# Kernel tuning notes

Hardware: AMD Instinct MI355X
Metric: run time of the kernel (lower is better)

Reference implementation:

```python
import jax, jax.numpy as jnp
import numpy as np

B, C, N = 8, 256, 2048
NMOD = 5  # time, space, time_cor, space_cor, global_res


def _attn(x, y, Wqk, Vw, Vb, Tw, Tb):
    """Offset self-attention (PCT-style). x, y: [B, C, N].
    q/k share the same 1x1-conv weight Wqk; v and trans convs have bias.
    softmax over last axis, then L1 renorm over axis=1 of the [B,N,N] map.
    """
    x_q = jnp.einsum('oc,bcn->bno', Wqk, y)           # [B,N,C]
    x_k = jnp.einsum('oc,bcn->bon', Wqk, x)           # [B,C,N]
    x_v = jnp.einsum('oc,bcn->bon', Vw, x) + Vb[:, None]
    att = jax.nn.softmax(jnp.einsum('bnc,bcm->bnm', x_q, x_k), axis=-1)
    att = att / (1e-07 + att.sum(axis=1, keepdims=True))
    x_r = jnp.einsum('bcn,bnm->bcm', x_v, att)        # [B,C,N]
    x_r = jax.nn.relu(jnp.einsum('oc,bcn->bon', Tw, x - x_r) + Tb[:, None])
    return x + x_r


def setup_inputs() -> dict:
    key = jax.random.key(0)
    ks = jax.random.split(key, 6)
    s = 1.0 / np.sqrt(C)
    return {
        'x':   jax.random.normal(ks[0], (B, 3, C, N), dtype=jnp.float32),
        'Wqk': jax.random.normal(ks[1], (NMOD, C, C), dtype=jnp.float32) * s,
        'Vw':  jax.random.normal(ks[2], (NMOD, C, C), dtype=jnp.float32) * s,
        'Vb':  jax.random.normal(ks[3], (NMOD, C), dtype=jnp.float32) * s,
        'Tw':  jax.random.normal(ks[4], (NMOD, C, C), dtype=jnp.float32) * s,
        'Tb':  jax.random.normal(ks[5], (NMOD, C), dtype=jnp.float32) * s,
    }


def reference(x, Wqk, Vw, Vb, Tw, Tb):
    time_x, mid, space_x = x[:, 0], x[:, 1], x[:, 2]

    def A(i, xx, yy):
        return _attn(xx, yy, Wqk[i], Vw[i], Vb[i], Tw[i], Tb[i])

    time_att = A(0, time_x, time_x)
    space_att = A(1, space_x, space_x)
    time_cor = A(2, time_x, space_x)
    space_cor = A(3, space_x, time_x)
    global_feat = A(4, mid, mid)

    time_update = jnp.tanh(time_att * jax.nn.sigmoid(time_cor))
    space_update = jnp.tanh(space_att * jax.nn.sigmoid(space_cor))
    g_sig = jax.nn.sigmoid(global_feat)
    global_residual = jax.nn.sigmoid(time_update * g_sig + space_update * g_sig)
    return mid + global_residual * jnp.tanh(global_feat)
```

## Files before the change

### kernel.cpp

```cpp
#include <hip/hip_runtime.h>
#include <math.h>

#define BB 8
#define CC 256
#define NN 2048

static const size_t NC  = (size_t)NN * CC;
static const size_t CN  = (size_t)CC * NN;

typedef unsigned short u16;
typedef __attribute__((ext_vector_type(8))) short short8;
typedef __attribute__((ext_vector_type(4))) float f32x4;

__device__ __forceinline__ float bf2f(u16 v) {
    union { unsigned int u; float f; } t; t.u = ((unsigned int)v) << 16; return t.f;
}
__device__ __forceinline__ u16 f2bf(float f) {
    union { float f; unsigned int u; } t; t.f = f;
    return (u16)((t.u + 0x7fffu + ((t.u >> 16) & 1u)) >> 16);
}
__device__ __forceinline__ float sigf(float x) { return 1.0f / (1.0f + expf(-x)); }

__device__ __forceinline__ size_t til(int r, int c, int tpr) {
    return (((size_t)((r >> 4) * tpr + (c >> 5))) << 9)
         + (size_t)((r & 15) << 5) + (size_t)(c & 31);
}

__device__ __forceinline__ void stage_tile(const u16* gtile, u16* ldst, int lane) {
    const u16* src = gtile + (lane & 15) * 32 + (lane >> 4) * 8;
    __builtin_amdgcn_global_load_lds(
        (const __attribute__((address_space(1))) void*)src,
        (__attribute__((address_space(3))) void*)ldst, 16, 0, 0);
}
#define WAITV(n) asm volatile("s_waitcnt vmcnt(" #n ")" ::: "memory")

__global__ __launch_bounds__(256) void cast_w(const float* __restrict__ in,
                                              u16* __restrict__ outp)
{
    const int mat = blockIdx.y;
    const int idx = blockIdx.x * 256 + threadIdx.x;
    const int c = idx >> 6, k = (idx & 63) << 2;
    const float4 v = *(const float4*)&in[(size_t)mat * (CC * CC) + (size_t)c * CC + k];
    ushort4 p;
    p.x = f2bf(v.x); p.y = f2bf(v.y); p.z = f2bf(v.z); p.w = f2bf(v.w);
    *(ushort4*)&outp[(size_t)mat * (CC * CC) + til(c, k, CC / 32)] = p;
}

__global__ __launch_bounds__(256) void tcast_x(const float* __restrict__ in,
                                               u16* __restrict__ out)
{
    const int z = blockIdx.z;
    const float* I = in + (size_t)z * CN;
    u16* O = out + (size_t)z * NC;
    const int c0 = blockIdx.y * 64, n0 = blockIdx.x * 64;
    const int tx = threadIdx.x & 15, ty = threadIdx.x >> 4;

    __shared__ float t[64][68];

    #pragma unroll
    for (int cc = 0; cc < 64; cc += 16) {
        const int c = ty + cc;
        *(float4*)&t[c][tx * 4] = *(const float4*)&I[(size_t)(c0 + c) * NN + n0 + tx * 4];
    }
    __syncthreads();
    #pragma unroll
    for (int nn2 = 0; nn2 < 64; nn2 += 16) {
        const int n = n0 + ty + nn2;
        const int c = c0 + tx * 4;
        ushort4 p;
        p.x = f2bf(t[tx * 4 + 0][ty + nn2]);
        p.y = f2bf(t[tx * 4 + 1][ty + nn2]);
        p.z = f2bf(t[tx * 4 + 2][ty + nn2]);
        p.w = f2bf(t[tx * 4 + 3][ty + nn2]);
        *(ushort4*)&O[til(n, c, 8)] = p;
    }
}

struct QkvP {
    const u16* w[12]; const u16* x[12]; u16* out[12];
    const float* bias[12]; int isv[12];
};

__global__ __launch_bounds__(256) void conv_qkv(QkvP P)
{
    const int z = blockIdx.z, job = z >> 3, b = z & 7;
    const int isv = P.isv[job];
    const u16* Wp = P.w[job];
    const u16* Xp = P.x[job] + (size_t)b * (3 * NC);
    const int n0 = blockIdx.x * 128, c0 = blockIdx.y * 128;
    const int lane = threadIdx.x & 63, wave = threadIdx.x >> 6;
    const int l15 = lane & 15, lg = lane >> 4;
    const int rA = (wave >> 1) * 64, rB = (wave & 1) * 64;

    const u16* Ab = isv ? Xp : Wp;
    const u16* Bb = isv ? Wp : Xp;
    const int Ar0 = (isv ? n0 : c0) + rA;
    const int Br0 = (isv ? c0 : n0) + rB;

    const u16* ap[4]; const u16* bp[4];
    #pragma unroll
    for (int i = 0; i < 4; i++) {
        ap[i] = Ab + til(Ar0 + i * 16 + l15, lg * 8, 8);
        bp[i] = Bb + til(Br0 + i * 16 + l15, lg * 8, 8);
    }

    f32x4 acc[4][4] = {};
    #pragma unroll 2
    for (int kc = 0; kc < 8; kc++) {
        short8 av[4], bv[4];
        #pragma unroll
        for (int i = 0; i < 4; i++) av[i] = *(const short8*)(ap[i] + kc * 512);
        #pragma unroll
        for (int i = 0; i < 4; i++) bv[i] = *(const short8*)(bp[i] + kc * 512);
        #pragma unroll
        for (int i = 0; i < 4; i++)
            #pragma unroll
            for (int j = 0; j < 4; j++)
                acc[i][j] = __builtin_amdgcn_mfma_f32_16x16x32_bf16(av[i], bv[j], acc[i][j], 0, 0, 0);
    }

    if (!isv) {
        u16* Ot = P.out[job] + (size_t)b * NC;
        #pragma unroll
        for (int i = 0; i < 4; i++) {
            const int c = c0 + rA + i * 16 + lg * 4;
            #pragma unroll
            for (int j = 0; j < 4; j++) {
                const int n = n0 + rB + j * 16 + l15;
                ushort4 p;
                p.x = f2bf(acc[i][j][0]); p.y = f2bf(acc[i][j][1]);
                p.z = f2bf(acc[i][j][2]); p.w = f2bf(acc[i][j][3]);
                *(ushort4*)&Ot[til(n, c, 8)] = p;
            }
        }
    } else {
        u16* Ov = P.out[job] + (size_t)b * CN;
        const float* bias = P.bias[job];
        #pragma unroll
        for (int j = 0; j < 4; j++) {
            const int c = c0 + rB + j * 16 + l15;
            const float bi = bias[c];
            #pragma unroll
            for (int i = 0; i < 4; i++) {
                const int n = n0 + rA + i * 16 + lg * 4;
                ushort4 p;
                p.x = f2bf(acc[i][j][0] + bi); p.y = f2bf(acc[i][j][1] + bi);
                p.z = f2bf(acc[i][j][2] + bi); p.w = f2bf(acc[i][j][3] + bi);
                *(ushort4*)&Ov[til(c, n, 64)] = p;
            }
        }
    }
}

__global__ __launch_bounds__(256) void conv_t2(
    const u16* __restrict__ W, const u16* __restrict__ Dt,
    const float* __restrict__ bias, const u16* __restrict__ Xts,
    u16* __restrict__ O)
{
    const int bid = blockIdx.x;
    const int b = bid & 7;
    const int rest = bid >> 3;
    const int cy = rest & 1, nx = rest >> 1;
    const int n0 = nx * 128, c0 = cy * 128;
    const int lane = threadIdx.x & 63, wave = threadIdx.x >> 6;
    const int l15 = lane & 15, lg = lane >> 4;
    const int wc = (wave >> 1) * 64, wn = (wave & 1) * 64;

    const u16* Xp = Dt + (size_t)b * NC;
    const u16* ap[4]; const u16* bp[4];
    #pragma unroll
    for (int i = 0; i < 4; i++) {
        ap[i] = W  + til(c0 + wc + i * 16 + l15, lg * 8, 8);
        bp[i] = Xp + til(n0 + wn + i * 16 + l15, lg * 8, 8);
    }

    f32x4 acc[4][4] = {};
    #pragma unroll 2
    for (int kc = 0; kc < 8; kc++) {
        short8 av[4], bv[4];
        #pragma unroll
        for (int i = 0; i < 4; i++) av[i] = *(const short8*)(ap[i] + kc * 512);
        #pragma unroll
        for (int i = 0; i < 4; i++) bv[i] = *(const short8*)(bp[i] + kc * 512);
        #pragma unroll
        for (int i = 0; i < 4; i++)
            #pragma unroll
            for (int j = 0; j < 4; j++)
                acc[i][j] = __builtin_amdgcn_mfma_f32_16x16x32_bf16(av[i], bv[j], acc[i][j], 0, 0, 0);
    }

    const u16* Xtb = Xts + (size_t)b * (3 * NC);
    u16* Ob = O + (size_t)b * CN;
    #pragma unroll
    for (int i = 0; i < 4; i++) {
        const int cb = c0 + wc + i * 16 + lg * 4;
        #pragma unroll
        for (int j = 0; j < 4; j++) {
            const int n = n0 + wn + j * 16 + l15;
            const ushort4 xv = *(const ushort4*)&Xtb[til(n, cb, 8)];
            const u16 xa[4] = { xv.x, xv.y, xv.z, xv.w };
            #pragma unroll
            for (int r = 0; r < 4; r++) {
                const int c = cb + r;
                const float v = bf2f(xa[r]) + fmaxf(acc[i][j][r] + bias[c], 0.0f);
                Ob[til(c, n, 64)] = f2bf(v);
            }
        }
    }
}

__global__ __launch_bounds__(1024) void attn_mfma6(
    const u16* __restrict__ Q, const u16* __restrict__ K,
    u16* __restrict__ Sout, float* __restrict__ CPb)
{
    const int bid = blockIdx.x;
    const int b = bid & 7;
    const int nblk = bid >> 3;
    const int n0 = nblk * 32;
    const int tid = threadIdx.x, lane = tid & 63, wave = tid >> 6;
    const int l15 = lane & 15, lg = lane >> 4;

    const u16* Qt = Q + (size_t)b * NC;
    const u16* Kt = K + (size_t)b * NC;

    __shared__ u16 KL[16 * 8 * 512];
    __shared__ u16 QL[16 * 512];
    __shared__ float red[16][32];
    __shared__ float rowstat[32];

    stage_tile(Qt + ((size_t)((n0 >> 4) + (wave >> 3)) * 8 + (wave & 7)) * 512,
               &QL[wave * 512], lane);
    u16* kw = &KL[wave * 4096];
    #pragma unroll
    for (int p = 0; p < 6; p++)
        stage_tile(Kt + ((size_t)(wave * 8 + (p & 7)) * 8 + (p >> 3)) * 512,
                   &kw[p * 512], lane);
    __syncthreads();

    f32x4 acc[2][8];
    #pragma unroll
    for (int g = 0; g < 2; g++)
        #pragma unroll
        for (int t = 0; t < 8; t++) acc[g][t] = (f32x4){0.f, 0.f, 0.f, 0.f};

    const int roff = lg * 128 + l15 * 8;

    #pragma unroll
    for (int kc = 0; kc < 8; kc++) {
        const short8 a0 = *(const short8*)&QL[kc * 512 + roff];
        const short8 a1 = *(const short8*)&QL[(8 + kc) * 512 + roff];
        #pragma unroll
        for (int t = 0; t < 8; t++) {
            const int i = kc * 8 + t;
            if (i < 58) { WAITV(5); } else if (i == 58) { WAITV(0); }
            const short8 bf = *(const short8*)&kw[(i & 7) * 512 + roff];
            if (i + 6 < 64) {
                const int j = i + 6;
                stage_tile(Kt + ((size_t)(wave * 8 + (j & 7)) * 8 + (j >> 3)) * 512,
                           &kw[(j & 7) * 512], lane);
            }
            __builtin_amdgcn_s_setprio(1);
            acc[0][t] = __builtin_amdgcn_mfma_f32_16x16x32_bf16(a0, bf, acc[0][t], 0, 0, 0);
            acc[1][t] = __builtin_amdgcn_mfma_f32_16x16x32_bf16(a1, bf, acc[1][t], 0, 0, 0);
            __builtin_amdgcn_s_setprio(0);
        }
    }

    float pm[2][4];
    #pragma unroll
    for (int g = 0; g < 2; g++)
        #pragma unroll
        for (int r = 0; r < 4; r++) {
            float m = acc[g][0][r];
            #pragma unroll
            for (int t = 1; t < 8; t++) m = fmaxf(m, acc[g][t][r]);
            #pragma unroll
            for (int o = 1; o <= 8; o <<= 1) m = fmaxf(m, __shfl_xor(m, o));
            pm[g][r] = m;
        }
    if (l15 == 0) {
        #pragma unroll
        for (int g = 0; g < 2; g++)
            #pragma unroll
            for (int r = 0; r < 4; r++) red[wave][g * 16 + lg * 4 + r] = pm[g][r];
    }
    __syncthreads();
    if (tid < 32) {
        float m = red[0][tid];
        #pragma unroll
        for (int w = 1; w < 16; w++) m = fmaxf(m, red[w][tid]);
        rowstat[tid] = m;
    }
    __syncthreads();

    float rm[2][4], ps[2][4];
    #pragma unroll
    for (int g = 0; g < 2; g++)
        #pragma unroll
        for (int r = 0; r < 4; r++) { rm[g][r] = rowstat[g * 16 + lg * 4 + r]; ps[g][r] = 0.f; }
    __syncthreads();

    #pragma unroll
    for (int g = 0; g < 2; g++)
        #pragma unroll
        for (int t = 0; t < 8; t++)
            #pragma unroll
            for (int r = 0; r < 4; r++) {
                const float e = __expf(acc[g][t][r] - rm[g][r]);
                acc[g][t][r] = e; ps[g][r] += e;
            }
    #pragma unroll
    for (int g = 0; g < 2; g++)
        #pragma unroll
        for (int r = 0; r < 4; r++)
            #pragma unroll
            for (int o = 1; o <= 8; o <<= 1) ps[g][r] += __shfl_xor(ps[g][r], o);
    if (l15 == 0) {
        #pragma unroll
        for (int g = 0; g < 2; g++)
            #pragma unroll
            for (int r = 0; r < 4; r++) red[wave][g * 16 + lg * 4 + r] = ps[g][r];
    }
    __syncthreads();
    if (tid < 32) {
        float s = red[0][tid];
        #pragma unroll
        for (int w = 1; w < 16; w++) s += red[w][tid];
        rowstat[tid] = 1.0f / s;
    }
    __syncthreads();

    float rv[2][4];
    #pragma unroll
    for (int g = 0; g < 2; g++)
        #pragma unroll
        for (int r = 0; r < 4; r++) rv[g][r] = rowstat[g * 16 + lg * 4 + r];

    u16* sb = Sout + (size_t)b * NN * NN;
    u16* sbg[2];
    #pragma unroll
    for (int g = 0; g < 2; g++)
        sbg[g] = sb + (size_t)((n0 >> 3) + g * 2 + (lg >> 1)) * (NN * 8) + (lg & 1) * 4;
    float* cpb = CPb + ((size_t)b * 64 + nblk) * NN;

    #pragma unroll
    for (int t = 0; t < 8; t++) {
        const int m = wave * 128 + t * 16 + l15;
        float cs = 0.0f;
        #pragma unroll
        for (int g = 0; g < 2; g++) {
            const float v0 = acc[g][t][0] * rv[g][0], v1 = acc[g][t][1] * rv[g][1];
            const float v2 = acc[g][t][2] * rv[g][2], v3 = acc[g][t][3] * rv[g][3];
            ushort4 pk;
            pk.x = f2bf(v0); pk.y = f2bf(v1); pk.z = f2bf(v2); pk.w = f2bf(v3);
            *(ushort4*)&sbg[g][(size_t)m * 8] = pk;
            cs += v0 + v1 + v2 + v3;
        }
        cs += __shfl_xor(cs, 16);
        cs += __shfl_xor(cs, 32);
        if (lane < 16) cpb[m] = cs;
    }
}

__global__ __launch_bounds__(256) void csum_kernel(const float* __restrict__ cp,
                                                   float* __restrict__ cs)
{
    const int b  = blockIdx.y;
    const int ml = threadIdx.x & 63;
    const int m  = blockIdx.x * 64 + ml;
    const int g0 = threadIdx.x >> 6;
    float s = 0.0f;
    for (int g = g0; g < 64; g += 4)
        s += cp[((size_t)b * 64 + g) * NN + m];
    __shared__ float red[4][64];
    red[g0][ml] = s;
    __syncthreads();
    if (threadIdx.x < 64) {
        cs[(size_t)b * NN + blockIdx.x * 64 + threadIdx.x] =
            red[0][threadIdx.x] + red[1][threadIdx.x] +
            red[2][threadIdx.x] + red[3][threadIdx.x];
    }
}

__global__ __launch_bounds__(256) void pv_mfma(
    const u16* __restrict__ V, const u16* __restrict__ S,
    const float* __restrict__ CSb, const u16* __restrict__ Xts,
    u16* __restrict__ DTo)
{
    const int bid = blockIdx.x;
    const int b = bid & 7;
    const int r2 = bid >> 3;
    const int cy = r2 & 1, mx = r2 >> 1;
    const int m0b = mx * 64, c0 = cy * 128;
    const int lane = threadIdx.x & 63, wave = threadIdx.x >> 6;
    const int wc = (wave >> 1) * 64, wm = (wave & 1) * 32;
    const int l15 = lane & 15, lg = lane >> 4;

    const u16* Vm = V + (size_t)b * CN;
    const u16* Sm = S + (size_t)b * NN * NN;

    f32x4 acc[4][2] = {};
    const u16* vp[4]; const u16* sp[2];
    #pragma unroll
    for (int ai = 0; ai < 4; ai++)
        vp[ai] = Vm + til(c0 + wc + ai * 16 + l15, lg * 8, 64);
    #pragma unroll
    for (int bj = 0; bj < 2; bj++)
        sp[bj] = Sm + ((size_t)lg * NN + m0b + wm + bj * 16 + l15) * 8;

    #pragma unroll 2
    for (int kc = 0; kc < 64; kc++) {
        short8 a[4], s2[2];
        #pragma unroll
        for (int ai = 0; ai < 4; ai++) { a[ai] = *(const short8*)vp[ai]; vp[ai] += 512; }
        #pragma unroll
        for (int bj = 0; bj < 2; bj++) { s2[bj] = *(const short8*)sp[bj]; sp[bj] += (size_t)4 * NN * 8; }
        #pragma unroll
        for (int ai = 0; ai < 4; ai++)
            #pragma unroll
            for (int bj = 0; bj < 2; bj++)
                acc[ai][bj] = __builtin_amdgcn_mfma_f32_16x16x32_bf16(a[ai], s2[bj], acc[ai][bj], 0, 0, 0);
    }

    const u16* Xtb = Xts + (size_t)b * (3 * NC);
    u16* Dtb = DTo + (size_t)b * NC;

    #pragma unroll
    for (int bj = 0; bj < 2; bj++) {
        const int m = m0b + wm + bj * 16 + l15;
        const float inv = 1.0f / (1e-7f + CSb[(size_t)b * NN + m]);
        #pragma unroll
        for (int ai = 0; ai < 4; ai++) {
            const int c = c0 + wc + ai * 16 + lg * 4;
            const size_t ad = til(m, c, 8);
            const ushort4 xv = *(const ushort4*)&Xtb[ad];
            ushort4 pk;
            pk.x = f2bf(bf2f(xv.x) - acc[ai][bj][0] * inv);
            pk.y = f2bf(bf2f(xv.y) - acc[ai][bj][1] * inv);
            pk.z = f2bf(bf2f(xv.z) - acc[ai][bj][2] * inv);
            pk.w = f2bf(bf2f(xv.w) - acc[ai][bj][3] * inv);
            *(ushort4*)&Dtb[ad] = pk;
        }
    }
}

__global__ __launch_bounds__(256) void ew_update_t(u16* __restrict__ A,
                                                   const u16* __restrict__ Bv)
{
    const size_t e = ((size_t)blockIdx.x * 256 + threadIdx.x) * 8;
    short8 a = *(const short8*)&A[e];
    const short8 b = *(const short8*)&Bv[e];
    #pragma unroll
    for (int j = 0; j < 8; j++) {
        const float f = tanhf(bf2f((u16)a[j]) * sigf(bf2f((u16)b[j])));
        a[j] = (short)f2bf(f);
    }
    *(short8*)&A[e] = a;
}

__global__ __launch_bounds__(256) void ew_final_t(
    const u16* __restrict__ TU, const u16* __restrict__ SU,
    const u16* __restrict__ G, const float* __restrict__ x,
    float* __restrict__ OUT)
{
    const size_t e = ((size_t)blockIdx.x * 256 + threadIdx.x) * 8;
    const int b = (int)(e / CN);
    const size_t r = e - (size_t)b * CN;
    const int tile = (int)(r >> 9), win = (int)(r & 511);
    const int row = win >> 5, col = win & 31;
    const int c = (tile >> 6) * 16 + row;
    const int n = (tile & 63) * 32 + col;

    const size_t lin = ((size_t)b * 3 + 1) * CN + (size_t)c * NN + n;
    const float4 m0 = *(const float4*)&x[lin];
    const float4 m1 = *(const float4*)&x[lin + 4];
    const float mid[8] = { m0.x, m0.y, m0.z, m0.w, m1.x, m1.y, m1.z, m1.w };

    const short8 tu = *(const short8*)&TU[e];
    const short8 su = *(const short8*)&SU[e];
    const short8 g  = *(const short8*)&G[e];

    float o[8];
    #pragma unroll
    for (int j = 0; j < 8; j++) {
        const float gg = bf2f((u16)g[j]);
        o[j] = mid[j] + sigf((bf2f((u16)tu[j]) + bf2f((u16)su[j])) * sigf(gg)) * tanhf(gg);
    }
    float* op = OUT + (size_t)b * CN + (size_t)c * NN + n;
    *(float4*)op       = (float4){o[0], o[1], o[2], o[3]};
    *(float4*)(op + 4) = (float4){o[4], o[5], o[6], o[7]};
}

extern "C" void kernel_launch(void* const* d_in, const int* in_sizes, int n_in,
                              void* d_out, int out_size, void* d_ws, size_t ws_size,
                              hipStream_t stream)
{
    const float* x   = (const float*)d_in[0];
    const float* Wqk = (const float*)d_in[1];
    const float* Vw  = (const float*)d_in[2];
    const float* VbF = (const float*)d_in[3];
    const float* Tw  = (const float*)d_in[4];
    const float* TbF = (const float*)d_in[5];
    float* out = (float*)d_out;

    const int mxs[5] = {0, 2, 0, 2, 1};
    const int mys[5] = {0, 2, 2, 0, 1};
    const int qjob[5] = {0, 1, 5, 6, 4};
    const int q_wi[7] = {0, 1, 2, 3, 4, 2, 3};
    const int q_xi[7] = {0, 2, 0, 2, 1, 2, 0};

    const size_t WSZ     = (size_t)CC * CC;
    const size_t QK_SLAB = (size_t)BB * NC;
    const size_t S_SLAB  = (size_t)BB * NN * NN;
    const size_t CP_SLAB = (size_t)BB * 64 * NN;
    const size_t CS_SLAB = (size_t)BB * NN;
    const size_t O_SLAB  = (size_t)BB * CN;

    const size_t base_b = 15 * WSZ * 2 + (size_t)BB * 3 * NC * 2;
    const size_t modtl  = S_SLAB * 2 + CP_SLAB * 4 + CS_SLAB * 4 + QK_SLAB * 2;
    const size_t margin = 2u << 20;
    const size_t need_1 = base_b + 12 * QK_SLAB * 2 + modtl + 3 * O_SLAB * 2 + margin;
    const size_t need_2 = base_b +  3 * QK_SLAB * 2 + modtl + 3 * O_SLAB * 2 + margin;

    const int tier2 = (ws_size >= need_1) ? 0 : 1;
    if (tier2 && ws_size < need_2) return;

    const int nQK = tier2 ? 2 : 7;
    const int nV  = tier2 ? 1 : 5;

    char* ws = (char*)d_ws;
    size_t off = 0;
    auto alloc = [&](size_t bytes) -> char* {
        char* p = ws + off; off += (bytes + 255) & ~255ULL; return p;
    };

    u16*   W16 = (u16*)  alloc(15 * WSZ * 2);
    u16*   Xt  = (u16*)  alloc((size_t)BB * 3 * NC * 2);
    u16*   QK  = (u16*)  alloc((size_t)nQK * QK_SLAB * 2);
    u16*   VB  = (u16*)  alloc((size_t)nV * QK_SLAB * 2);
    u16*   S   = (u16*)  alloc(S_SLAB * 2);
    float* CP  = (float*)alloc(CP_SLAB * 4);
    float* CS  = (float*)alloc(CS_SLAB * 4);
    u16*   DT  = (u16*)  alloc(QK_SLAB * 2);
    u16*   OB  = (u16*)  alloc(3 * O_SLAB * 2);

    cast_w<<<dim3(64, 5), 256, 0, stream>>>(Wqk, W16);
    cast_w<<<dim3(64, 5), 256, 0, stream>>>(Vw,  W16 + 5 * WSZ);
    cast_w<<<dim3(64, 5), 256, 0, stream>>>(Tw,  W16 + 10 * WSZ);
    tcast_x<<<dim3(NN / 64, CC / 64, BB * 3), 256, 0, stream>>>(x, Xt);

    if (!tier2) {
        QkvP qp{};
        for (int j = 0; j < 7; j++) {
            qp.w[j] = W16 + (size_t)q_wi[j] * WSZ;
            qp.x[j] = Xt + (size_t)q_xi[j] * NC;
            qp.out[j] = QK + (size_t)j * QK_SLAB;
            qp.isv[j] = 0; qp.bias[j] = nullptr;
        }
        for (int i = 0; i < 5; i++) {
            const int j = 7 + i;
            qp.w[j] = W16 + (size_t)(5 + i) * WSZ;
            qp.x[j] = Xt + (size_t)mxs[i] * NC;
            qp.out[j] = VB + (size_t)i * QK_SLAB;
            qp.isv[j] = 1; qp.bias[j] = VbF + (size_t)i * CC;
        }
        conv_qkv<<<dim3(NN / 128, CC / 128, 96), 256, 0, stream>>>(qp);
    }

    auto run_mod = [&](int i, u16* O) {
        const u16* Qp; const u16* Kp; const u16* Vp;
        if (!tier2) {
            Qp = QK + (size_t)qjob[i] * QK_SLAB;
            Kp = QK + (size_t)i * QK_SLAB;
            Vp = VB + (size_t)i * QK_SLAB;
        } else {
            QkvP qp{}; int nj = 0;
            qp.w[nj] = W16 + (size_t)i * WSZ; qp.x[nj] = Xt + (size_t)mxs[i] * NC;
            qp.out[nj] = QK; qp.isv[nj] = 0; nj++;
            Qp = QK; Kp = QK;
            if (mys[i] != mxs[i]) {
                qp.w[nj] = W16 + (size_t)i * WSZ; qp.x[nj] = Xt + (size_t)mys[i] * NC;
                qp.out[nj] = QK + QK_SLAB; qp.isv[nj] = 0; nj++;
                Qp = QK + QK_SLAB;
            }
            qp.w[nj] = W16 + (size_t)(5 + i) * WSZ; qp.x[nj] = Xt + (size_t)mxs[i] * NC;
            qp.out[nj] = VB; qp.isv[nj] = 1; qp.bias[nj] = VbF + (size_t)i * CC; nj++;
            conv_qkv<<<dim3(NN / 128, CC / 128, 8 * nj), 256, 0, stream>>>(qp);
            Vp = VB;
        }
        attn_mfma6<<<512, 1024, 0, stream>>>(Qp, Kp, S, CP);
        csum_kernel<<<dim3(NN / 64, BB), 256, 0, stream>>>(CP, CS);
        pv_mfma<<<512, 256, 0, stream>>>(Vp, S, CS, Xt + (size_t)mxs[i] * NC, DT);
        conv_t2<<<256, 256, 0, stream>>>(W16 + (size_t)(10 + i) * WSZ, DT,
                                         TbF + (size_t)i * CC,
                                         Xt + (size_t)mxs[i] * NC, O);
    };

    u16* OB0 = OB;
    u16* OB1 = OB + O_SLAB;
    u16* OB2 = OB + 2 * O_SLAB;
    const int ewg = (int)(((size_t)BB * CN) / (256 * 8));

    run_mod(0, OB0);
    run_mod(2, OB1);
    ew_update_t<<<ewg, 256, 0, stream>>>(OB0, OB1);
    run_mod(1, OB1);
    run_mod(3, OB2);
    ew_update_t<<<ewg, 256, 0, stream>>>(OB1, OB2);
    run_mod(4, OB2);
    ew_final_t<<<ewg, 256, 0, stream>>>(OB0, OB1, OB2, x, out);
}
```

Baseline: 648.6 us.

## Recompute attention scores in PV kernel instead of materializing the bf16 score matrix

The first attention pass now stores only the per-row max and inverse sum, and no longer writes the full B×N×N bf16 softmax matrix. The PV kernel recomputes QK^T per 32-column chunk with MFMA, applies exp and the row statistics, stages the tile in shared memory, and multiplies by V. This removes a 64MB-per-module write and read of S. In exchange the QK^T matmul runs twice, the grid is halved to 256 blocks of 512 threads, and each chunk adds two block barriers.

Result: slower. 1.141 ms (+75.9%).

```diff
diff --git a/kernel.cpp b/kernel.cpp
--- a/kernel.cpp
+++ b/kernel.cpp
@@ -209,9 +209,9 @@
     }
 }
 
-__global__ __launch_bounds__(1024) void attn_mfma6(
+__global__ __launch_bounds__(1024) void attn_pass1(
     const u16* __restrict__ Q, const u16* __restrict__ K,
-    u16* __restrict__ Sout, float* __restrict__ CPb)
+    float* __restrict__ RSg, float* __restrict__ CPb)
 {
     const int bid = blockIdx.x;
     const int b = bid & 7;
@@ -290,6 +290,7 @@
         #pragma unroll
         for (int w = 1; w < 16; w++) m = fmaxf(m, red[w][tid]);
         rowstat[tid] = m;
+        RSg[((size_t)b * NN + n0 + tid) * 2] = m;
     }
     __syncthreads();
 
@@ -326,7 +327,9 @@
         float s = red[0][tid];
         #pragma unroll
         for (int w = 1; w < 16; w++) s += red[w][tid];
-        rowstat[tid] = 1.0f / s;
+        const float inv = 1.0f / s;
+        rowstat[tid] = inv;
+        RSg[((size_t)b * NN + n0 + tid) * 2 + 1] = inv;
     }
     __syncthreads();
 
@@ -336,26 +339,15 @@
         #pragma unroll
         for (int r = 0; r < 4; r++) rv[g][r] = rowstat[g * 16 + lg * 4 + r];
 
-    u16* sb = Sout + (size_t)b * NN * NN;
-    u16* sbg[2];
-    #pragma unroll
-    for (int g = 0; g < 2; g++)
-        sbg[g] = sb + (size_t)((n0 >> 3) + g * 2 + (lg >> 1)) * (NN * 8) + (lg & 1) * 4;
     float* cpb = CPb + ((size_t)b * 64 + nblk) * NN;
-
     #pragma unroll
     for (int t = 0; t < 8; t++) {
         const int m = wave * 128 + t * 16 + l15;
         float cs = 0.0f;
         #pragma unroll
-        for (int g = 0; g < 2; g++) {
-            const float v0 = acc[g][t][0] * rv[g][0], v1 = acc[g][t][1] * rv[g][1];
-            const float v2 = acc[g][t][2] * rv[g][2], v3 = acc[g][t][3] * rv[g][3];
-            ushort4 pk;
-            pk.x = f2bf(v0); pk.y = f2bf(v1); pk.z = f2bf(v2); pk.w = f2bf(v3);
-            *(ushort4*)&sbg[g][(size_t)m * 8] = pk;
-            cs += v0 + v1 + v2 + v3;
-        }
+        for (int g = 0; g < 2; g++)
+            cs += acc[g][t][0] * rv[g][0] + acc[g][t][1] * rv[g][1]
+                + acc[g][t][2] * rv[g][2] + acc[g][t][3] * rv[g][3];
         cs += __shfl_xor(cs, 16);
         cs += __shfl_xor(cs, 32);
         if (lane < 16) cpb[m] = cs;
@@ -382,56 +374,98 @@
     }
 }
 
-__global__ __launch_bounds__(256) void pv_mfma(
-    const u16* __restrict__ V, const u16* __restrict__ S,
+__global__ __launch_bounds__(512) void pv_fuse(
+    const u16* __restrict__ Q, const u16* __restrict__ K,
+    const u16* __restrict__ V, const float* __restrict__ RSg,
     const float* __restrict__ CSb, const u16* __restrict__ Xts,
     u16* __restrict__ DTo)
 {
     const int bid = blockIdx.x;
     const int b = bid & 7;
-    const int r2 = bid >> 3;
-    const int cy = r2 & 1, mx = r2 >> 1;
-    const int m0b = mx * 64, c0 = cy * 128;
-    const int lane = threadIdx.x & 63, wave = threadIdx.x >> 6;
-    const int wc = (wave >> 1) * 64, wm = (wave & 1) * 32;
-    const int l15 = lane & 15, lg = lane >> 4;
-
+    const int mx = bid >> 3;
+    const int m0 = mx * 64;
+    const int tid = threadIdx.x, lane = tid & 63, wave = tid >> 6;
+    const int l15 = lane & 15, lg = lane >> 4, rb = lg * 4;
+    const int wn2 = wave >> 2, wm4 = wave & 3;
+    const int wc4 = wave >> 1, wm2 = wave & 1;
+
+    const u16* Qt = Q + (size_t)b * NC;
+    const u16* Kt = K + (size_t)b * NC;
     const u16* Vm = V + (size_t)b * CN;
-    const u16* Sm = S + (size_t)b * NN * NN;
+
+    __shared__ u16 KT[32 * 512];
+    __shared__ u16 SB[64 * 40];
+    __shared__ float2 rsl[NN];
+    __shared__ float csl[64];
+
+    #pragma unroll
+    for (int j = 0; j < 4; j++) {
+        const int t = wave * 4 + j;
+        stage_tile(Kt + ((size_t)((mx * 4 + (t >> 3)) * 8) + (t & 7)) * 512,
+                   &KT[t * 512], lane);
+    }
+    for (int k = tid; k < NN; k += 512)
+        rsl[k] = ((const float2*)RSg)[(size_t)b * NN + k];
+    if (tid < 64) csl[tid] = 1.0f / (1e-7f + CSb[(size_t)b * NN + m0 + tid]);
+    __syncthreads();
+
+    const int roff = lg * 128 + l15 * 8;
+    const int sbw = (wm4 * 16 + l15) * 40 + wn2 * 16 + rb;
+    const int sbr = (wm2 * 32 + l15) * 40 + lg * 8;
 
     f32x4 acc[4][2] = {};
-    const u16* vp[4]; const u16* sp[2];
-    #pragma unroll
-    for (int ai = 0; ai < 4; ai++)
-        vp[ai] = Vm + til(c0 + wc + ai * 16 + l15, lg * 8, 64);
-    #pragma unroll
-    for (int bj = 0; bj < 2; bj++)
-        sp[bj] = Sm + ((size_t)lg * NN + m0b + wm + bj * 16 + l15) * 8;
-
-    #pragma unroll 2
-    for (int kc = 0; kc < 64; kc++) {
-        short8 a[4], s2[2];
-        #pragma unroll
-        for (int ai = 0; ai < 4; ai++) { a[ai] = *(const short8*)vp[ai]; vp[ai] += 512; }
-        #pragma unroll
-        for (int bj = 0; bj < 2; bj++) { s2[bj] = *(const short8*)sp[bj]; sp[bj] += (size_t)4 * NN * 8; }
+
+    for (int ch = 0; ch < 64; ch++) {
+        const int n0c = ch * 32 + wn2 * 16;
+        const u16* qb = Qt + ((size_t)(n0c >> 4) * 8) * 512 + l15 * 32 + lg * 8;
+        f32x4 qk = (f32x4){0.f, 0.f, 0.f, 0.f};
+        #pragma unroll
+        for (int kc = 0; kc < 8; kc++) {
+            const short8 a  = *(const short8*)(qb + kc * 512);
+            const short8 bf = *(const short8*)&KT[(wm4 * 8 + kc) * 512 + roff];
+            qk = __builtin_amdgcn_mfma_f32_16x16x32_bf16(a, bf, qk, 0, 0, 0);
+        }
+        ushort4 pk;
+        {
+            const float2 s0 = rsl[n0c + rb + 0];
+            const float2 s1 = rsl[n0c + rb + 1];
+            const float2 s2 = rsl[n0c + rb + 2];
+            const float2 s3 = rsl[n0c + rb + 3];
+            pk.x = f2bf(__expf(qk[0] - s0.x) * s0.y);
+            pk.y = f2bf(__expf(qk[1] - s1.x) * s1.y);
+            pk.z = f2bf(__expf(qk[2] - s2.x) * s2.y);
+            pk.w = f2bf(__expf(qk[3] - s3.x) * s3.y);
+        }
+        *(ushort4*)&SB[sbw] = pk;
+        __syncthreads();
+
+        short8 vf[4], sf[2];
         #pragma unroll
         for (int ai = 0; ai < 4; ai++)
+            vf[ai] = *(const short8*)(Vm + til(wc4 * 64 + ai * 16 + l15,
+                                               ch * 32 + lg * 8, 64));
+        #pragma unroll
+        for (int bj = 0; bj < 2; bj++)
+            sf[bj] = *(const short8*)&SB[sbr + bj * 16 * 40];
+        #pragma unroll
+        for (int ai = 0; ai < 4; ai++)
             #pragma unroll
             for (int bj = 0; bj < 2; bj++)
-                acc[ai][bj] = __builtin_amdgcn_mfma_f32_16x16x32_bf16(a[ai], s2[bj], acc[ai][bj], 0, 0, 0);
+                acc[ai][bj] = __builtin_amdgcn_mfma_f32_16x16x32_bf16(
+                                  vf[ai], sf[bj], acc[ai][bj], 0, 0, 0);
+        __syncthreads();
     }
 
     const u16* Xtb = Xts + (size_t)b * (3 * NC);
     u16* Dtb = DTo + (size_t)b * NC;
-
     #pragma unroll
     for (int bj = 0; bj < 2; bj++) {
-        const int m = m0b + wm + bj * 16 + l15;
-        const float inv = 1.0f / (1e-7f + CSb[(size_t)b * NN + m]);
+        const int mloc = wm2 * 32 + bj * 16 + l15;
+        const int m = m0 + mloc;
+        const float inv = csl[mloc];
         #pragma unroll
         for (int ai = 0; ai < 4; ai++) {
-            const int c = c0 + wc + ai * 16 + lg * 4;
+            const int c = wc4 * 64 + ai * 16 + rb;
             const size_t ad = til(m, c, 8);
             const ushort4 xv = *(const ushort4*)&Xtb[ad];
             ushort4 pk;
@@ -511,13 +545,13 @@
 
     const size_t WSZ     = (size_t)CC * CC;
     const size_t QK_SLAB = (size_t)BB * NC;
-    const size_t S_SLAB  = (size_t)BB * NN * NN;
     const size_t CP_SLAB = (size_t)BB * 64 * NN;
     const size_t CS_SLAB = (size_t)BB * NN;
+    const size_t RS_SLAB = (size_t)BB * NN * 2;
     const size_t O_SLAB  = (size_t)BB * CN;
 
     const size_t base_b = 15 * WSZ * 2 + (size_t)BB * 3 * NC * 2;
-    const size_t modtl  = S_SLAB * 2 + CP_SLAB * 4 + CS_SLAB * 4 + QK_SLAB * 2;
+    const size_t modtl  = CP_SLAB * 4 + CS_SLAB * 4 + RS_SLAB * 4 + QK_SLAB * 2;
     const size_t margin = 2u << 20;
     const size_t need_1 = base_b + 12 * QK_SLAB * 2 + modtl + 3 * O_SLAB * 2 + margin;
     const size_t need_2 = base_b +  3 * QK_SLAB * 2 + modtl + 3 * O_SLAB * 2 + margin;
@@ -538,9 +572,9 @@
     u16*   Xt  = (u16*)  alloc((size_t)BB * 3 * NC * 2);
     u16*   QK  = (u16*)  alloc((size_t)nQK * QK_SLAB * 2);
     u16*   VB  = (u16*)  alloc((size_t)nV * QK_SLAB * 2);
-    u16*   S   = (u16*)  alloc(S_SLAB * 2);
     float* CP  = (float*)alloc(CP_SLAB * 4);
     float* CS  = (float*)alloc(CS_SLAB * 4);
+    float* RS  = (float*)alloc(RS_SLAB * 4);
     u16*   DT  = (u16*)  alloc(QK_SLAB * 2);
     u16*   OB  = (u16*)  alloc(3 * O_SLAB * 2);
 
@@ -588,9 +622,10 @@
             conv_qkv<<<dim3(NN / 128, CC / 128, 8 * nj), 256, 0, stream>>>(qp);
             Vp = VB;
         }
-        attn_mfma6<<<512, 1024, 0, stream>>>(Qp, Kp, S, CP);
+        attn_pass1<<<512, 1024, 0, stream>>>(Qp, Kp, RS, CP);
         csum_kernel<<<dim3(NN / 64, BB), 256, 0, stream>>>(CP, CS);
-        pv_mfma<<<512, 256, 0, stream>>>(Vp, S, CS, Xt + (size_t)mxs[i] * NC, DT);
+        pv_fuse<<<256, 512, 0, stream>>>(Qp, Kp, Vp, RS, CS,
+                                         Xt + (size_t)mxs[i] * NC, DT);
         conv_t2<<<256, 256, 0, stream>>>(W16 + (size_t)(10 + i) * WSZ, DT,
                                          TbF + (size_t)i * CC,
                                          Xt + (size_t)mxs[i] * NC, O);
```

## Double-buffer conv_qkv operand tiles through per-wave LDS ring with async staging

Applied to the files above, without the earlier changes.

conv_qkv now stages A/B operand tiles into a per-wave two-slot LDS ring using stage_tile (presumably direct global-to-LDS loads) two k-steps ahead, waiting on vmcnt before reading fragments. This replaces the direct global short8 loads in the MFMA loop and is meant to hide global memory latency behind the MFMA work. It also raises wave priority around the MFMA block. The cost is 64KB of LDS per block, which may limit occupancy, plus the extra LDS traffic.

After: 643.2 us (median of 2 runs). Within noise of the previous version (-0.8%).

```diff
diff --git a/kernel.cpp b/kernel.cpp
--- a/kernel.cpp
+++ b/kernel.cpp
@@ -97,26 +97,45 @@
     const int Ar0 = (isv ? n0 : c0) + rA;
     const int Br0 = (isv ? c0 : n0) + rB;
 
-    const u16* ap[4]; const u16* bp[4];
-    #pragma unroll
-    for (int i = 0; i < 4; i++) {
-        ap[i] = Ab + til(Ar0 + i * 16 + l15, lg * 8, 8);
-        bp[i] = Bb + til(Br0 + i * 16 + l15, lg * 8, 8);
-    }
-
+    __shared__ u16 ring[4][16][512];
+    u16* rw = &ring[wave][0][0];
+
+    auto stage8 = [&](int kc, int grp) {
+        #pragma unroll
+        for (int i = 0; i < 4; i++)
+            stage_tile(Ab + ((size_t)((Ar0 >> 4) + i) * 8 + kc) * 512,
+                       rw + (size_t)(grp + i) * 512, lane);
+        #pragma unroll
+        for (int i = 0; i < 4; i++)
+            stage_tile(Bb + ((size_t)((Br0 >> 4) + i) * 8 + kc) * 512,
+                       rw + (size_t)(grp + 4 + i) * 512, lane);
+    };
+
+    stage8(0, 0);
+    stage8(1, 8);
+
+    const int roff = lg * 128 + l15 * 8;
     f32x4 acc[4][4] = {};
-    #pragma unroll 2
+
+    #pragma unroll
     for (int kc = 0; kc < 8; kc++) {
+        if (kc < 7) { WAITV(8); } else { WAITV(0); }
+        const int g = (kc & 1) * 8;
         short8 av[4], bv[4];
         #pragma unroll
-        for (int i = 0; i < 4; i++) av[i] = *(const short8*)(ap[i] + kc * 512);
-        #pragma unroll
-        for (int i = 0; i < 4; i++) bv[i] = *(const short8*)(bp[i] + kc * 512);
+        for (int i = 0; i < 4; i++) av[i] = *(const short8*)&rw[(size_t)(g + i) * 512 + roff];
+        #pragma unroll
+        for (int i = 0; i < 4; i++) bv[i] = *(const short8*)&rw[(size_t)(g + 4 + i) * 512 + roff];
+        asm volatile("s_waitcnt lgkmcnt(0)" ::: "memory");
+        __builtin_amdgcn_sched_barrier(0);
+        if (kc + 2 < 8) stage8(kc + 2, g);
+        __builtin_amdgcn_s_setprio(1);
         #pragma unroll
         for (int i = 0; i < 4; i++)
             #pragma unroll
             for (int j = 0; j < 4; j++)
                 acc[i][j] = __builtin_amdgcn_mfma_f32_16x16x32_bf16(av[i], bv[j], acc[i][j], 0, 0, 0);
+        __builtin_amdgcn_s_setprio(0);
     }
 
     if (!isv) {
```
